# Optimization experiments

Measured on AMD Instinct MI355X. Metric: run time of the kernel, lower is better.

The kernel has to match this reference:

```python
import jax, jax.numpy as jnp
from jax import lax
import numpy as np
import math

IMPOSSIBLE = -10000.0
B, S, D_MODEL, TAG = 64, 1024, 512, 48

def setup_inputs():
    key = jax.random.key(0)
    k1, k2, k3, k4 = jax.random.split(key, 4)
    feature_vec = jax.random.normal(k1, (B, S, D_MODEL), jnp.float32)
    y = jax.random.randint(k2, (B, S), 0, TAG, dtype=jnp.int32)
    mask = jnp.zeros((B, S), dtype=bool)  # True = pad
    W = jax.random.normal(k3, (TAG, D_MODEL), jnp.float32) / math.sqrt(D_MODEL)  # feature2tag weight (out,in)
    transition = jax.random.normal(k4, (TAG + 2, TAG + 2), jnp.float32)
    transition = transition.at[:, TAG].set(IMPOSSIBLE).at[TAG + 1, :].set(IMPOSSIBLE)
    return {"feature_vec": feature_vec, "y": y, "mask": mask, "W": W, "transition": transition}

def _loss(feature_vec, W, transition, y, mask):
    b, s, d = feature_vec.shape
    t = W.shape[0]
    tag_vec = jnp.einsum('bsd,td->bst', feature_vec, W) / jnp.sqrt(jnp.float32(d))
    bm = (~mask).astype(tag_vec.dtype)                 # 1 where valid, 0 where pad
    L = (s - mask.sum(-1) - 1).astype(jnp.int32)       # last valid position per batch
    start = transition[t]                              # row SRT_IDX
    end = transition[:, t + 1]                         # col END_IDX
    trans_tt = transition[:t, :t]

    # ----- gold path score S(X, y) (fully vectorized over time) -----
    ysafe = jnp.where(mask, 0, y)
    emit = jnp.take_along_axis(tag_vec, ysafe[..., None], axis=2)[..., 0] * bm  # (b,s)
    score = start[y[:, 0]] + emit.sum(-1)
    score = score + (transition[y[:, :-1], y[:, 1:]] * bm[:, 1:]).sum(-1)
    end_tok = jnp.take_along_axis(y, L[:, None], axis=1)[:, 0]
    score = score + end[end_tok]

    # ----- log partition: forward algorithm as a fused scan over seq_len -----
    bm_next = jnp.concatenate([bm[:, 1:], jnp.zeros((b, 1), bm.dtype)], axis=1)
    def fstep(prev, inp):
        e, m0, m1 = inp  # (b,t), (b,), (b,)
        sc = (prev + e * m0[:, None])[:, :, None] + trans_tt[None] * m1[:, None, None]  # (b,t,t)
        return jax.nn.logsumexp(sc, axis=1), None
    prev0 = jnp.broadcast_to(start[:t], (b, t))
    prev, _ = lax.scan(fstep, prev0, (tag_vec.transpose(1, 0, 2), bm.T, bm_next.T))
    logZ = jax.nn.logsumexp(prev + end[:t][None], axis=-1)
    return logZ - score, tag_vec, L, trans_tt, start, end

def _viterbi(tag_vec, L, trans_tt, start, end):
    b, s, t = tag_vec.shape
    def vstep(prev, e):  # prev: (b,t,t) prev-tag x cur-tag scores; e: (b,t)
        sc = prev + e[:, None, :]
        best = sc.max(axis=1)
        idx = sc.argmax(axis=1).astype(jnp.int32)
        return best[:, :, None] + trans_tt, (best, idx)
    prev0 = jnp.broadcast_to(start[:t][None, None, :], (b, t, t))
    _, (stage_score, stage_idx) = lax.scan(vstep, prev0, tag_vec.transpose(1, 0, 2))  # (s,b,t) each
    final = stage_score[L, jnp.arange(b)] + end[:t][None]  # (b,t) scores at last valid step
    now0 = final.argmax(axis=1).astype(jnp.int32)
    # backtrace as reverse scan; padded positions emit -1
    js = jnp.arange(s - 1, 0, -1, dtype=jnp.int32)
    idx_rev = stage_idx[1:][::-1]  # step j = s-1 .. 1
    def bstep(now, inp):
        idx_j, j = inp
        prev_tag = jnp.take_along_axis(idx_j, now[:, None], axis=1)[:, 0]
        active = j <= L
        return jnp.where(active, prev_tag, now), jnp.where(active, prev_tag, -1)
    _, outs = lax.scan(bstep, now0, (idx_rev, js))  # (s-1, b): tag at position j-1
    path = jnp.concatenate([outs[::-1].T, jnp.full((b, 1), -1, jnp.int32)], axis=1)  # (b,s)
    path = path.at[jnp.arange(b), L].set(now0)
    return path

def reference(feature_vec, y, mask, W, transition):
    loss, tag_vec, L, trans_tt, start, end = _loss(feature_vec, W, transition, y, mask)
    path = _viterbi(tag_vec, L, trans_tt, start, end)
    return loss, path
```

## Files before the change

kernel.cpp:

```cpp
#include <hip/hip_runtime.h>

#define B_ 64
#define S_ 1024
#define NT 48
#define DM 512
#define TT 50

typedef float v2f __attribute__((ext_vector_type(2)));
typedef float v4f __attribute__((ext_vector_type(4)));

__global__ __launch_bounds__(256) void k_tagvec(const float* __restrict__ F,
                                                const float* __restrict__ Wm,
                                                float* __restrict__ out) {
  __shared__ float fs[128][68];
  __shared__ float wsh[48][68];
  const int t = threadIdx.x;
  const int rowBase = blockIdx.x * 128;
  const int jg = t & 3;
  const int rq = t >> 2;
  const int r0 = rq * 2, r1 = r0 + 1;
  float acc0[12];
  float acc1[12];
#pragma unroll
  for (int q = 0; q < 12; ++q) { acc0[q] = 0.f; acc1[q] = 0.f; }
  for (int kc = 0; kc < DM; kc += 64) {
    __syncthreads();
#pragma unroll
    for (int i2 = 0; i2 < 8; ++i2) {
      int f = t + i2 * 256;
      int row = f >> 4, kk = f & 15;
      float4 v = *(const float4*)(F + (size_t)(rowBase + row) * DM + kc + kk * 4);
      *(float4*)&fs[row][kk * 4] = v;
    }
#pragma unroll
    for (int i2 = 0; i2 < 3; ++i2) {
      int f = t + i2 * 256;
      int row = f >> 4, kk = f & 15;
      float4 v = *(const float4*)(Wm + (size_t)row * DM + kc + kk * 4);
      *(float4*)&wsh[row][kk * 4] = v;
    }
    __syncthreads();
#pragma unroll 4
    for (int k4 = 0; k4 < 16; ++k4) {
      float4 a0 = *(const float4*)&fs[r0][k4 * 4];
      float4 a1 = *(const float4*)&fs[r1][k4 * 4];
#pragma unroll
      for (int jj = 0; jj < 12; ++jj) {
        float4 w = *(const float4*)&wsh[jg * 12 + jj][k4 * 4];
        acc0[jj] += a0.x * w.x + a0.y * w.y + a0.z * w.z + a0.w * w.w;
        acc1[jj] += a1.x * w.x + a1.y * w.y + a1.z * w.z + a1.w * w.w;
      }
    }
  }
  const float sc = 0.044194173824159216f;
  size_t base0 = (size_t)(rowBase + r0) * NT + jg * 12;
  size_t base1 = (size_t)(rowBase + r1) * NT + jg * 12;
#pragma unroll
  for (int q = 0; q < 3; ++q) {
    float4 o0 = make_float4(acc0[q*4]*sc, acc0[q*4+1]*sc, acc0[q*4+2]*sc, acc0[q*4+3]*sc);
    float4 o1 = make_float4(acc1[q*4]*sc, acc1[q*4+1]*sc, acc1[q*4+2]*sc, acc1[q*4+3]*sc);
    *(float4*)(out + base0 + q*4) = o0;
    *(float4*)(out + base1 + q*4) = o1;
  }
}

__global__ __launch_bounds__(256) void k_score(const float* __restrict__ tg,
                                               const int* __restrict__ y,
                                               const unsigned char* __restrict__ mask,
                                               const float* __restrict__ trans,
                                               float* __restrict__ scoreOut) {
  const int b = blockIdx.x, t = threadIdx.x;
  const int* yb = y + (size_t)b * S_;
  const unsigned char* mbp = mask + (size_t)b * S_;
  float part = 0.f;
  int cnt = 0;
  for (int s = t; s < S_; s += 256) {
    int ys = yb[s];
    int ms = mbp[s];
    float bm = ms ? 0.f : 1.f;
    int yy = ms ? 0 : ys;
    part += tg[((size_t)b * S_ + s) * NT + yy] * bm;
    if (s >= 1) part += trans[yb[s - 1] * TT + ys] * bm;
    cnt += ms ? 1 : 0;
  }
  for (int d = 1; d < 64; d <<= 1) {
    part += __shfl_xor(part, d);
    cnt += __shfl_xor(cnt, d);
  }
  __shared__ float pw[4];
  __shared__ int cw[4];
  int wid = t >> 6;
  if ((t & 63) == 0) { pw[wid] = part; cw[wid] = cnt; }
  __syncthreads();
  if (t == 0) {
    float tot = pw[0] + pw[1] + pw[2] + pw[3];
    int c = cw[0] + cw[1] + cw[2] + cw[3];
    int L = S_ - 1 - c;
    tot += trans[NT * TT + yb[0]];
    tot += trans[yb[L] * TT + (NT + 1)];
    scoreOut[b] = tot;
  }
}

__global__ __launch_bounds__(64, 1) void k_scan(const float* __restrict__ tg,
                                                const unsigned char* __restrict__ mask,
                                                const float* __restrict__ trans,
                                                const float* __restrict__ score,
                                                float* __restrict__ Mbuf,
                                                int* __restrict__ nowbuf,
                                                float* __restrict__ out) {
  alignas(16) __shared__ float pls[64];
  __shared__ float bmL[S_ + 8];
  __shared__ float rbuf[256];

  const int t = threadIdx.x;
  const bool isV = blockIdx.x >= B_;
  const int b = isV ? (blockIdx.x - B_) : blockIdx.x;
  const int jc = (t < NT) ? t : (NT - 1);
  const float* tgb = tg + (size_t)b * S_ * NT;

  int cnt = 0;
  for (int m = t; m < S_; m += 64) {
    unsigned char mv = mask[(size_t)b * S_ + m];
    bmL[m] = mv ? 0.f : 1.f;
    cnt += mv ? 1 : 0;
  }
  if (t < 8) bmL[S_ + t] = 0.f;
#pragma unroll
  for (int d = 1; d < 64; d <<= 1) cnt += __shfl_xor(cnt, d);
  const int L = S_ - 1 - cnt;
  __syncthreads();

  if (!isV) {
    v2f E2[24];
#pragma unroll
    for (int q = 0; q < 24; ++q) {
      E2[q].x = __expf(trans[(2 * q) * TT + jc]);
      E2[q].y = __expf(trans[(2 * q + 1) * TT + jc]);
    }
    pls[t] = __expf(trans[NT * TT + jc] + tgb[jc] * bmL[0]);
    float ebuf[8];
#pragma unroll
    for (int k = 0; k < 8; ++k) ebuf[k] = tgb[(size_t)(k + 1) * NT + jc];
    const float* ebp = tgb + (size_t)9 * NT + jc;
    float pfinal = 0.f;

#define FSTEP(KK, RENORM, DOREFILL)                                            \
    {                                                                          \
      v4f bb4[12];                                                             \
      _Pragma("unroll")                                                        \
      for (int q = 0; q < 12; ++q) bb4[q] = *(const v4f*)&pls[4 * q];          \
      const v2f* bb = (const v2f*)bb4;                                         \
      float m1r = bmp[KK];                                                     \
      int m1b = __builtin_amdgcn_readfirstlane(__float_as_int(m1r));           \
      float Z;                                                                 \
      if (m1b != 0) {                                                          \
        v2f z0 = bb[0] * E2[0], z1 = bb[1] * E2[1];                            \
        v2f z2 = bb[2] * E2[2], z3 = bb[3] * E2[3];                            \
        _Pragma("unroll")                                                      \
        for (int q = 4; q < 24; q += 4) {                                      \
          z0 = __builtin_elementwise_fma(bb[q + 0], E2[q + 0], z0);            \
          z1 = __builtin_elementwise_fma(bb[q + 1], E2[q + 1], z1);            \
          z2 = __builtin_elementwise_fma(bb[q + 2], E2[q + 2], z2);            \
          z3 = __builtin_elementwise_fma(bb[q + 3], E2[q + 3], z3);            \
        }                                                                      \
        v2f zz = (z0 + z1) + (z2 + z3);                                        \
        Z = zz.x + zz.y;                                                       \
      } else {                                                                 \
        v2f z0 = bb[0] + bb[1], z1 = bb[2] + bb[3];                            \
        v2f z2 = bb[4] + bb[5], z3 = bb[6] + bb[7];                            \
        _Pragma("unroll")                                                      \
        for (int q = 8; q < 24; q += 4) {                                      \
          z0 = z0 + bb[q + 0]; z1 = z1 + bb[q + 1];                            \
          z2 = z2 + bb[q + 2]; z3 = z3 + bb[q + 3];                            \
        }                                                                      \
        v2f zz = (z0 + z1) + (z2 + z3);                                        \
        Z = zz.x + zz.y;                                                       \
      }                                                                        \
      float pnew = Z;                                                          \
      if (RENORM) {                                                            \
        float s48[48];                                                         \
        _Pragma("unroll")                                                      \
        for (int q = 0; q < 24; ++q) { s48[2 * q] = bb[q].x; s48[2 * q + 1] = bb[q].y; } \
        float m16[16];                                                         \
        _Pragma("unroll")                                                      \
        for (int q = 0; q < 16; ++q)                                           \
          m16[q] = fmaxf(fmaxf(s48[3 * q], s48[3 * q + 1]), s48[3 * q + 2]);   \
        float u0 = fmaxf(fmaxf(m16[0], m16[1]), m16[2]);                       \
        float u1 = fmaxf(fmaxf(m16[3], m16[4]), m16[5]);                       \
        float u2 = fmaxf(fmaxf(m16[6], m16[7]), m16[8]);                       \
        float u3 = fmaxf(fmaxf(m16[9], m16[10]), m16[11]);                     \
        float u4 = fmaxf(fmaxf(m16[12], m16[13]), m16[14]);                    \
        float w0 = fmaxf(fmaxf(u0, u1), u2);                                   \
        float w1 = fmaxf(fmaxf(u3, u4), m16[15]);                              \
        float M = fmaxf(w0, w1);                                               \
        float r = __builtin_amdgcn_rcpf(M);                                    \
        pnew = Z * r;                                                          \
        if (t == 0) rbuf[2 * g + (KK >> 2)] = r;                               \
      }                                                                        \
      float pe = pnew * __expf(ebuf[KK] * m1r);                                \
      pls[t] = pe;                                                             \
      if (DOREFILL) ebuf[KK] = ebp[KK * NT];                                   \
    }

    {
      const float* bmp = &bmL[1];
      for (int g = 0; g < 127; ++g) {
        const bool rf = (g < 126);
        FSTEP(0, 0, 1) FSTEP(1, 0, 1) FSTEP(2, 0, 1) FSTEP(3, 1, 1)
        FSTEP(4, 0, 1) FSTEP(5, 0, 1) FSTEP(6, 0, 1)
        if (rf) { FSTEP(7, 1, 1) } else { FSTEP(7, 1, 0) }
        ebp += 8 * NT;
        bmp += 8;
      }
      {
        const int g = 127;
        FSTEP(0, 0, 0) FSTEP(1, 0, 0) FSTEP(2, 0, 0) FSTEP(3, 1, 0)
        FSTEP(4, 0, 0) FSTEP(5, 0, 0) FSTEP(6, 0, 0)
      }
    }
#undef FSTEP
    {
      v4f bb4[12];
#pragma unroll
      for (int q = 0; q < 12; ++q) bb4[q] = *(const v4f*)&pls[4 * q];
      const v2f* bb = (const v2f*)bb4;
      v2f z0 = bb[0] + bb[1], z1 = bb[2] + bb[3];
      v2f z2 = bb[4] + bb[5], z3 = bb[6] + bb[7];
#pragma unroll
      for (int q = 8; q < 24; q += 4) {
        z0 = z0 + bb[q + 0]; z1 = z1 + bb[q + 1];
        z2 = z2 + bb[q + 2]; z3 = z3 + bb[q + 3];
      }
      v2f zz = (z0 + z1) + (z2 + z3);
      float Z = zz.x + zz.y;
      float s48[48];
#pragma unroll
      for (int q = 0; q < 24; ++q) { s48[2 * q] = bb[q].x; s48[2 * q + 1] = bb[q].y; }
      float m16[16];
#pragma unroll
      for (int q = 0; q < 16; ++q)
        m16[q] = fmaxf(fmaxf(s48[3 * q], s48[3 * q + 1]), s48[3 * q + 2]);
      float u0 = fmaxf(fmaxf(m16[0], m16[1]), m16[2]);
      float u1 = fmaxf(fmaxf(m16[3], m16[4]), m16[5]);
      float u2 = fmaxf(fmaxf(m16[6], m16[7]), m16[8]);
      float u3 = fmaxf(fmaxf(m16[9], m16[10]), m16[11]);
      float u4 = fmaxf(fmaxf(m16[12], m16[13]), m16[14]);
      float w0 = fmaxf(fmaxf(u0, u1), u2);
      float w1 = fmaxf(fmaxf(u3, u4), m16[15]);
      float M = fmaxf(w0, w1);
      float r = __builtin_amdgcn_rcpf(M);
      if (t == 0) rbuf[255] = r;
      pfinal = Z * r;
    }
    float ls = 0.f;
#pragma unroll
    for (int k = 0; k < 4; ++k) ls += __logf(rbuf[t + 64 * k]);
#pragma unroll
    for (int d = 1; d < 64; d <<= 1) ls += __shfl_xor(ls, d);
    float v = (t < NT) ? pfinal * __expf(trans[t * TT + (NT + 1)]) : 0.f;
#pragma unroll
    for (int d = 1; d < 64; d <<= 1) v += __shfl_xor(v, d);
    if (t == 0) out[b] = __logf(v) - ls - score[b];
  } else {
    v2f T2[24];
#pragma unroll
    for (int q = 0; q < 24; ++q) {
      T2[q].x = trans[(2 * q) * TT + jc];
      T2[q].y = trans[(2 * q + 1) * TT + jc];
    }
    float* Mb = Mbuf + (size_t)b * S_ * NT;
    const float best0 = trans[NT * TT + jc] + tgb[jc];
    pls[t] = best0;
    float ebuf[8];
#pragma unroll
    for (int k = 0; k < 8; ++k) ebuf[k] = tgb[(size_t)(1 + k) * NT + jc];
    const float* ebp = tgb + (size_t)9 * NT + jc;
    float* mbp = Mb + NT + jc;

#define VSTEP(KK, DOREFILL)                                                    \
    {                                                                          \
      v4f bb4[12];                                                             \
      _Pragma("unroll")                                                        \
      for (int q = 0; q < 12; ++q) bb4[q] = *(const v4f*)&pls[4 * q];          \
      const v2f* bb = (const v2f*)bb4;                                         \
      v2f c2[24];                                                              \
      _Pragma("unroll")                                                        \
      for (int q = 0; q < 24; ++q) c2[q] = bb[q] + T2[q];                      \
      float s48[48];                                                           \
      _Pragma("unroll")                                                        \
      for (int q = 0; q < 24; ++q) { s48[2 * q] = c2[q].x; s48[2 * q + 1] = c2[q].y; } \
      float m16[16];                                                           \
      _Pragma("unroll")                                                        \
      for (int q = 0; q < 16; ++q)                                             \
        m16[q] = fmaxf(fmaxf(s48[3 * q], s48[3 * q + 1]), s48[3 * q + 2]);     \
      float u0 = fmaxf(fmaxf(m16[0], m16[1]), m16[2]);                         \
      float u1 = fmaxf(fmaxf(m16[3], m16[4]), m16[5]);                         \
      float u2 = fmaxf(fmaxf(m16[6], m16[7]), m16[8]);                         \
      float u3 = fmaxf(fmaxf(m16[9], m16[10]), m16[11]);                       \
      float u4 = fmaxf(fmaxf(m16[12], m16[13]), m16[14]);                      \
      float w0 = fmaxf(fmaxf(u0, u1), u2);                                     \
      float w1 = fmaxf(fmaxf(u3, u4), m16[15]);                                \
      float M = fmaxf(w0, w1);                                                 \
      mbp[KK * NT] = M;                                                        \
      float bnew = M + ebuf[KK];                                               \
      pls[t] = bnew;                                                           \
      if (DOREFILL) ebuf[KK] = ebp[KK * NT];                                   \
    }

    for (int g = 0; g < 127; ++g) {
      const bool rf = (g < 126);
      VSTEP(0, 1) VSTEP(1, 1) VSTEP(2, 1) VSTEP(3, 1)
      VSTEP(4, 1) VSTEP(5, 1) VSTEP(6, 1)
      if (rf) { VSTEP(7, 1) } else { VSTEP(7, 0) }
      mbp += 8 * NT;
      ebp += 8 * NT;
    }
    VSTEP(0, 0) VSTEP(1, 0) VSTEP(2, 0) VSTEP(3, 0)
    VSTEP(4, 0) VSTEP(5, 0) VSTEP(6, 0)
#undef VSTEP
    float fin;
    if (L > 0) {
      fin = Mb[(size_t)L * NT + jc] + tgb[(size_t)L * NT + jc];
    } else {
      fin = best0;
    }
    float v = (t < NT) ? (fin + trans[t * TT + (NT + 1)]) : -3.0e38f;
    float M = v;
#pragma unroll
    for (int d = 1; d < 64; d <<= 1) M = fmaxf(M, __shfl_xor(M, d));
    unsigned long long ball = __ballot(v == M);
    int now0 = __ffsll(ball) - 1;
    if (t == 0) nowbuf[b] = now0;
  }
}

__global__ __launch_bounds__(256) void k_idx(const float* __restrict__ tg,
                                             const float* __restrict__ Mbuf,
                                             const float* __restrict__ trans,
                                             unsigned char* __restrict__ idxbuf) {
  __shared__ float TshT[NT][NT];
  const int t = threadIdx.x;
  const int b = blockIdx.x;
  for (int k = t; k < NT * NT; k += 256) {
    int i = k / NT, j = k - i * NT;
    TshT[j][i] = trans[i * TT + j];
  }
  __syncthreads();
  const int s = blockIdx.y * 128 + (t >> 1);
  const int jh = (t & 1) * 24;
  if (s < 1) return;
  const float* tgb = tg + (size_t)b * S_ * NT;
  const float* Mb = Mbuf + (size_t)b * S_ * NT;
  float bprev[NT];
  if (s == 1) {
#pragma unroll
    for (int i = 0; i < NT; ++i) bprev[i] = trans[NT * TT + i] + tgb[i];
  } else {
#pragma unroll
    for (int i = 0; i < NT; ++i)
      bprev[i] = Mb[(size_t)(s - 1) * NT + i] + tgb[(size_t)(s - 1) * NT + i];
  }
  unsigned char* ob = idxbuf + ((size_t)b * S_ + s) * NT + jh;
#pragma unroll 4
  for (int jj = 0; jj < 24; ++jj) {
    int j = jh + jj;
    float M = Mb[(size_t)s * NT + j];
    int idx = 0;
#pragma unroll
    for (int i = NT - 1; i >= 0; --i) {
      float cc = bprev[i] + TshT[j][i];
      idx = (cc == M) ? i : idx;
    }
    ob[jj] = (unsigned char)idx;
  }
}

__global__ __launch_bounds__(1024) void k_btrack(const unsigned char* __restrict__ idxbuf,
                                                 const unsigned char* __restrict__ mask,
                                                 const int* __restrict__ nowbuf,
                                                 float* __restrict__ out) {
  __shared__ unsigned char idxL[S_][NT];
  __shared__ unsigned char mapc[16][NT];
  __shared__ int ELs[16];
  __shared__ int cnt_sh;
  const int t = threadIdx.x;
  const int b = blockIdx.x;
  if (t == 0) cnt_sh = 0;
  __syncthreads();
  {
    const unsigned int* src = (const unsigned int*)(idxbuf + (size_t)b * S_ * NT);
    unsigned int* dst = (unsigned int*)&idxL[t][0];
#pragma unroll
    for (int k = 0; k < 12; ++k) dst[k] = src[(size_t)t * 12 + k];
  }
  int mv = mask[(size_t)b * S_ + t] ? 1 : 0;
  unsigned long long bal = __ballot(mv);
  int wcnt = __popcll(bal);
  if ((t & 63) == 0 && wcnt) atomicAdd(&cnt_sh, wcnt);
  __syncthreads();
  const int L = S_ - 1 - cnt_sh;
  const int now0 = nowbuf[b];
  if (t < 16 * NT) {
    const int c = t / NT;
    const int g = t - c * NT;
    int cur = g;
    const int top = (c == 15) ? (S_ - 1) : (c + 1) * 64;
    const int base = c * 64;
    for (int m = top; m > base; --m) {
      if (m <= L) cur = idxL[m][cur];
    }
    mapc[c][g] = (unsigned char)cur;
  }
  __syncthreads();
  if (t == 0) {
    int e = now0;
    ELs[15] = e;
    for (int c2 = 15; c2 >= 1; --c2) {
      e = mapc[c2][e];
      ELs[c2 - 1] = e;
    }
  }
  __syncthreads();
  float* pathOut = out + B_ + (size_t)b * S_;
  if (t < 16) {
    const int c = t;
    const int top = (c == 15) ? (S_ - 1) : (c + 1) * 64;
    const int base = c * 64;
    int cu = ELs[c];
    for (int m = top; m > base; --m) {
      if (m <= L) cu = idxL[m][cu];
      int pos = m - 1;
      pathOut[pos] = (pos > L) ? -1.0f : (float)cu;
    }
  }
  if (t == 0) pathOut[S_ - 1] = (L == S_ - 1) ? (float)now0 : -1.0f;
}

extern "C" void kernel_launch(void* const* d_in, const int* in_sizes, int n_in,
                              void* d_out, int out_size, void* d_ws, size_t ws_size,
                              hipStream_t stream) {
  const float* F = (const float*)d_in[0];
  const int* y = (const int*)d_in[1];
  const unsigned char* mask = (const unsigned char*)d_in[2];
  const float* Wm = (const float*)d_in[3];
  const float* trans = (const float*)d_in[4];
  float* out = (float*)d_out;

  const size_t NTG = (size_t)B_ * S_ * NT;
  float* tg = (float*)d_ws;
  float* score = tg + NTG;
  float* Mbuf = score + 64;
  int* nowbuf = (int*)(Mbuf + NTG);
  unsigned char* idxbuf = (unsigned char*)(nowbuf + 64);

  k_tagvec<<<dim3((B_ * S_) / 128), dim3(256), 0, stream>>>(F, Wm, tg);
  k_score<<<dim3(B_), dim3(256), 0, stream>>>(tg, y, mask, trans, score);
  k_scan<<<dim3(2 * B_), dim3(64), 0, stream>>>(tg, mask, trans, score, Mbuf, nowbuf, out);
  k_idx<<<dim3(B_, 8), dim3(256), 0, stream>>>(tg, Mbuf, trans, idxbuf);
  k_btrack<<<dim3(B_), dim3(1024), 0, stream>>>(idxbuf, mask, nowbuf, out);
}
```

Measured before the change: 318.0 us.

## Fuse gold-path score into forward scan and hoist emission loads in steps

```diff
diff --git a/kernel.cpp b/kernel.cpp
--- a/kernel.cpp
+++ b/kernel.cpp
@@ -64,61 +64,53 @@
   }
 }
 
-__global__ __launch_bounds__(256) void k_score(const float* __restrict__ tg,
-                                               const int* __restrict__ y,
-                                               const unsigned char* __restrict__ mask,
-                                               const float* __restrict__ trans,
-                                               float* __restrict__ scoreOut) {
-  const int b = blockIdx.x, t = threadIdx.x;
-  const int* yb = y + (size_t)b * S_;
-  const unsigned char* mbp = mask + (size_t)b * S_;
-  float part = 0.f;
-  int cnt = 0;
-  for (int s = t; s < S_; s += 256) {
-    int ys = yb[s];
-    int ms = mbp[s];
-    float bm = ms ? 0.f : 1.f;
-    int yy = ms ? 0 : ys;
-    part += tg[((size_t)b * S_ + s) * NT + yy] * bm;
-    if (s >= 1) part += trans[yb[s - 1] * TT + ys] * bm;
-    cnt += ms ? 1 : 0;
-  }
-  for (int d = 1; d < 64; d <<= 1) {
-    part += __shfl_xor(part, d);
-    cnt += __shfl_xor(cnt, d);
-  }
-  __shared__ float pw[4];
-  __shared__ int cw[4];
-  int wid = t >> 6;
-  if ((t & 63) == 0) { pw[wid] = part; cw[wid] = cnt; }
-  __syncthreads();
-  if (t == 0) {
-    float tot = pw[0] + pw[1] + pw[2] + pw[3];
-    int c = cw[0] + cw[1] + cw[2] + cw[3];
-    int L = S_ - 1 - c;
-    tot += trans[NT * TT + yb[0]];
-    tot += trans[yb[L] * TT + (NT + 1)];
-    scoreOut[b] = tot;
-  }
-}
-
-__global__ __launch_bounds__(64, 1) void k_scan(const float* __restrict__ tg,
-                                                const unsigned char* __restrict__ mask,
-                                                const float* __restrict__ trans,
-                                                const float* __restrict__ score,
-                                                float* __restrict__ Mbuf,
-                                                int* __restrict__ nowbuf,
-                                                float* __restrict__ out) {
+__global__ __launch_bounds__(128, 1) void k_scan(const float* __restrict__ tg,
+                                                 const int* __restrict__ y,
+                                                 const unsigned char* __restrict__ mask,
+                                                 const float* __restrict__ trans,
+                                                 float* __restrict__ Mbuf,
+                                                 int* __restrict__ nowbuf,
+                                                 float* __restrict__ out) {
   alignas(16) __shared__ float pls[64];
   __shared__ float bmL[S_ + 8];
   __shared__ float rbuf[256];
+  __shared__ float sc_lds;
 
   const int t = threadIdx.x;
   const bool isV = blockIdx.x >= B_;
   const int b = isV ? (blockIdx.x - B_) : blockIdx.x;
+  const float* tgb = tg + (size_t)b * S_ * NT;
+
+  if (t >= 64) {
+    if (!isV) {
+      const int* yb = y + (size_t)b * S_;
+      const unsigned char* mbp2 = mask + (size_t)b * S_;
+      float part = 0.f;
+      int cnt = 0;
+      for (int s = t - 64; s < S_; s += 64) {
+        int ys = yb[s];
+        int ms = mbp2[s];
+        float bm = ms ? 0.f : 1.f;
+        int yy = ms ? 0 : ys;
+        part += tgb[(size_t)s * NT + yy] * bm;
+        if (s >= 1) part += trans[yb[s - 1] * TT + ys] * bm;
+        cnt += ms ? 1 : 0;
+      }
+#pragma unroll
+      for (int d = 1; d < 64; d <<= 1) {
+        part += __shfl_xor(part, d);
+        cnt += __shfl_xor(cnt, d);
+      }
+      if ((t & 63) == 0) {
+        int L2 = S_ - 1 - cnt;
+        sc_lds = part + trans[NT * TT + yb[0]] + trans[yb[L2] * TT + (NT + 1)];
+      }
+    }
+    __syncthreads();
+    return;
+  }
+
   const int jc = (t < NT) ? t : (NT - 1);
-  const float* tgb = tg + (size_t)b * S_ * NT;
-
   int cnt = 0;
   for (int m = t; m < S_; m += 64) {
     unsigned char mv = mask[(size_t)b * S_ + m];
@@ -150,6 +142,8 @@
       v4f bb4[12];                                                             \
       _Pragma("unroll")                                                        \
       for (int q = 0; q < 12; ++q) bb4[q] = *(const v4f*)&pls[4 * q];          \
+      float ev = ebuf[KK];                                                     \
+      if (DOREFILL) ebuf[KK] = ebp[KK * NT];  \
       const v2f* bb = (const v2f*)bb4;                                         \
       float m1r = bmp[KK];                                                     \
       int m1b = __builtin_amdgcn_readfirstlane(__float_as_int(m1r));           \
@@ -198,9 +192,8 @@
         pnew = Z * r;                                                          \
         if (t == 0) rbuf[2 * g + (KK >> 2)] = r;                               \
       }                                                                        \
-      float pe = pnew * __expf(ebuf[KK] * m1r);                                \
+      float pe = pnew * __expf(ev * m1r);                                      \
       pls[t] = pe;                                                             \
-      if (DOREFILL) ebuf[KK] = ebp[KK * NT];                                   \
     }
 
     {
@@ -215,6 +208,7 @@
       }
       {
         const int g = 127;
+        const float* bmp = &bmL[1017];
         FSTEP(0, 0, 0) FSTEP(1, 0, 0) FSTEP(2, 0, 0) FSTEP(3, 1, 0)
         FSTEP(4, 0, 0) FSTEP(5, 0, 0) FSTEP(6, 0, 0)
       }
@@ -261,7 +255,7 @@
     float v = (t < NT) ? pfinal * __expf(trans[t * TT + (NT + 1)]) : 0.f;
 #pragma unroll
     for (int d = 1; d < 64; d <<= 1) v += __shfl_xor(v, d);
-    if (t == 0) out[b] = __logf(v) - ls - score[b];
+    if (t == 0) out[b] = __logf(v) - ls - sc_lds;
   } else {
     v2f T2[24];
 #pragma unroll
@@ -272,6 +266,7 @@
     float* Mb = Mbuf + (size_t)b * S_ * NT;
     const float best0 = trans[NT * TT + jc] + tgb[jc];
     pls[t] = best0;
+    float Mprev = best0;
     float ebuf[8];
 #pragma unroll
     for (int k = 0; k < 8; ++k) ebuf[k] = tgb[(size_t)(1 + k) * NT + jc];
@@ -283,6 +278,9 @@
       v4f bb4[12];                                                             \
       _Pragma("unroll")                                                        \
       for (int q = 0; q < 12; ++q) bb4[q] = *(const v4f*)&pls[4 * q];          \
+      mbp[(KK - 1) * NT] = Mprev;               \
+      float ev = ebuf[KK];                                                     \
+      if (DOREFILL) ebuf[KK] = ebp[KK * NT];           \
       const v2f* bb = (const v2f*)bb4;                                         \
       v2f c2[24];                                                              \
       _Pragma("unroll")                                                        \
@@ -302,10 +300,9 @@
       float w0 = fmaxf(fmaxf(u0, u1), u2);                                     \
       float w1 = fmaxf(fmaxf(u3, u4), m16[15]);                                \
       float M = fmaxf(w0, w1);                                                 \
-      mbp[KK * NT] = M;                                                        \
-      float bnew = M + ebuf[KK];                                               \
+      float bnew = M + ev;                                                     \
       pls[t] = bnew;                                                           \
-      if (DOREFILL) ebuf[KK] = ebp[KK * NT];                                   \
+      Mprev = M;                                                               \
     }
 
     for (int g = 0; g < 127; ++g) {
@@ -319,6 +316,7 @@
     VSTEP(0, 0) VSTEP(1, 0) VSTEP(2, 0) VSTEP(3, 0)
     VSTEP(4, 0) VSTEP(5, 0) VSTEP(6, 0)
 #undef VSTEP
+    mbp[6 * NT] = Mprev;
     float fin;
     if (L > 0) {
       fin = Mb[(size_t)L * NT + jc] + tgb[(size_t)L * NT + jc];
@@ -449,14 +447,12 @@
 
   const size_t NTG = (size_t)B_ * S_ * NT;
   float* tg = (float*)d_ws;
-  float* score = tg + NTG;
-  float* Mbuf = score + 64;
+  float* Mbuf = tg + NTG;
   int* nowbuf = (int*)(Mbuf + NTG);
   unsigned char* idxbuf = (unsigned char*)(nowbuf + 64);
 
   k_tagvec<<<dim3((B_ * S_) / 128), dim3(256), 0, stream>>>(F, Wm, tg);
-  k_score<<<dim3(B_), dim3(256), 0, stream>>>(tg, y, mask, trans, score);
-  k_scan<<<dim3(2 * B_), dim3(64), 0, stream>>>(tg, mask, trans, score, Mbuf, nowbuf, out);
+  k_scan<<<dim3(2 * B_), dim3(128), 0, stream>>>(tg, y, mask, trans, Mbuf, nowbuf, out);
   k_idx<<<dim3(B_, 8), dim3(256), 0, stream>>>(tg, Mbuf, trans, idxbuf);
   k_btrack<<<dim3(B_), dim3(1024), 0, stream>>>(idxbuf, mask, nowbuf, out);
 }
```

New measurement: 325.2 us. 1.02x slower.

## Fuse gold-score, argmax-index and backtrack kernels into one per-batch kernel

Applied to the files above, without the earlier changes.

```diff
diff --git a/kernel.cpp b/kernel.cpp
--- a/kernel.cpp
+++ b/kernel.cpp
@@ -64,48 +64,9 @@
   }
 }
 
-__global__ __launch_bounds__(256) void k_score(const float* __restrict__ tg,
-                                               const int* __restrict__ y,
-                                               const unsigned char* __restrict__ mask,
-                                               const float* __restrict__ trans,
-                                               float* __restrict__ scoreOut) {
-  const int b = blockIdx.x, t = threadIdx.x;
-  const int* yb = y + (size_t)b * S_;
-  const unsigned char* mbp = mask + (size_t)b * S_;
-  float part = 0.f;
-  int cnt = 0;
-  for (int s = t; s < S_; s += 256) {
-    int ys = yb[s];
-    int ms = mbp[s];
-    float bm = ms ? 0.f : 1.f;
-    int yy = ms ? 0 : ys;
-    part += tg[((size_t)b * S_ + s) * NT + yy] * bm;
-    if (s >= 1) part += trans[yb[s - 1] * TT + ys] * bm;
-    cnt += ms ? 1 : 0;
-  }
-  for (int d = 1; d < 64; d <<= 1) {
-    part += __shfl_xor(part, d);
-    cnt += __shfl_xor(cnt, d);
-  }
-  __shared__ float pw[4];
-  __shared__ int cw[4];
-  int wid = t >> 6;
-  if ((t & 63) == 0) { pw[wid] = part; cw[wid] = cnt; }
-  __syncthreads();
-  if (t == 0) {
-    float tot = pw[0] + pw[1] + pw[2] + pw[3];
-    int c = cw[0] + cw[1] + cw[2] + cw[3];
-    int L = S_ - 1 - c;
-    tot += trans[NT * TT + yb[0]];
-    tot += trans[yb[L] * TT + (NT + 1)];
-    scoreOut[b] = tot;
-  }
-}
-
 __global__ __launch_bounds__(64, 1) void k_scan(const float* __restrict__ tg,
                                                 const unsigned char* __restrict__ mask,
                                                 const float* __restrict__ trans,
-                                                const float* __restrict__ score,
                                                 float* __restrict__ Mbuf,
                                                 int* __restrict__ nowbuf,
                                                 float* __restrict__ out) {
@@ -261,7 +222,7 @@
     float v = (t < NT) ? pfinal * __expf(trans[t * TT + (NT + 1)]) : 0.f;
 #pragma unroll
     for (int d = 1; d < 64; d <<= 1) v += __shfl_xor(v, d);
-    if (t == 0) out[b] = __logf(v) - ls - score[b];
+    if (t == 0) out[b] = __logf(v) - ls;
   } else {
     v2f T2[24];
 #pragma unroll
@@ -335,69 +296,102 @@
   }
 }
 
-__global__ __launch_bounds__(256) void k_idx(const float* __restrict__ tg,
-                                             const float* __restrict__ Mbuf,
-                                             const float* __restrict__ trans,
-                                             unsigned char* __restrict__ idxbuf) {
+__global__ __launch_bounds__(1024) void k_idxbt(const float* __restrict__ tg,
+                                                const float* __restrict__ Mbuf,
+                                                const int* __restrict__ y,
+                                                const unsigned char* __restrict__ mask,
+                                                const float* __restrict__ trans,
+                                                const int* __restrict__ nowbuf,
+                                                float* __restrict__ out) {
   __shared__ float TshT[NT][NT];
-  const int t = threadIdx.x;
-  const int b = blockIdx.x;
-  for (int k = t; k < NT * NT; k += 256) {
-    int i = k / NT, j = k - i * NT;
-    TshT[j][i] = trans[i * TT + j];
-  }
-  __syncthreads();
-  const int s = blockIdx.y * 128 + (t >> 1);
-  const int jh = (t & 1) * 24;
-  if (s < 1) return;
-  const float* tgb = tg + (size_t)b * S_ * NT;
-  const float* Mb = Mbuf + (size_t)b * S_ * NT;
-  float bprev[NT];
-  if (s == 1) {
-#pragma unroll
-    for (int i = 0; i < NT; ++i) bprev[i] = trans[NT * TT + i] + tgb[i];
-  } else {
-#pragma unroll
-    for (int i = 0; i < NT; ++i)
-      bprev[i] = Mb[(size_t)(s - 1) * NT + i] + tgb[(size_t)(s - 1) * NT + i];
-  }
-  unsigned char* ob = idxbuf + ((size_t)b * S_ + s) * NT + jh;
-#pragma unroll 4
-  for (int jj = 0; jj < 24; ++jj) {
-    int j = jh + jj;
-    float M = Mb[(size_t)s * NT + j];
-    int idx = 0;
-#pragma unroll
-    for (int i = NT - 1; i >= 0; --i) {
-      float cc = bprev[i] + TshT[j][i];
-      idx = (cc == M) ? i : idx;
-    }
-    ob[jj] = (unsigned char)idx;
-  }
-}
-
-__global__ __launch_bounds__(1024) void k_btrack(const unsigned char* __restrict__ idxbuf,
-                                                 const unsigned char* __restrict__ mask,
-                                                 const int* __restrict__ nowbuf,
-                                                 float* __restrict__ out) {
   __shared__ unsigned char idxL[S_][NT];
   __shared__ unsigned char mapc[16][NT];
   __shared__ int ELs[16];
   __shared__ int cnt_sh;
+  __shared__ float pw[4];
+  __shared__ int cw[4];
+  __shared__ float sc_sh;
+
   const int t = threadIdx.x;
   const int b = blockIdx.x;
+  const float* tgb = tg + (size_t)b * S_ * NT;
+  const float* Mb = Mbuf + (size_t)b * S_ * NT;
   if (t == 0) cnt_sh = 0;
-  __syncthreads();
-  {
-    const unsigned int* src = (const unsigned int*)(idxbuf + (size_t)b * S_ * NT);
-    unsigned int* dst = (unsigned int*)&idxL[t][0];
-#pragma unroll
-    for (int k = 0; k < 12; ++k) dst[k] = src[(size_t)t * 12 + k];
+  for (int k = t; k < NT * NT; k += 1024) {
+    int i = k / NT, j = k - i * NT;
+    TshT[j][i] = trans[i * TT + j];
   }
   int mv = mask[(size_t)b * S_ + t] ? 1 : 0;
   unsigned long long bal = __ballot(mv);
   int wcnt = __popcll(bal);
   if ((t & 63) == 0 && wcnt) atomicAdd(&cnt_sh, wcnt);
+  if (t < 256) {
+    const int* yb = y + (size_t)b * S_;
+    const unsigned char* mbp = mask + (size_t)b * S_;
+    float part = 0.f;
+    int cnt = 0;
+    for (int s = t; s < S_; s += 256) {
+      int ys = yb[s];
+      int ms = mbp[s];
+      float bm = ms ? 0.f : 1.f;
+      int yy = ms ? 0 : ys;
+      part += tgb[(size_t)s * NT + yy] * bm;
+      if (s >= 1) part += trans[yb[s - 1] * TT + ys] * bm;
+      cnt += ms ? 1 : 0;
+    }
+#pragma unroll
+    for (int d = 1; d < 64; d <<= 1) {
+      part += __shfl_xor(part, d);
+      cnt += __shfl_xor(cnt, d);
+    }
+    int wid = t >> 6;
+    if ((t & 63) == 0) { pw[wid] = part; cw[wid] = cnt; }
+  }
+  __syncthreads();
+  if (t == 0) {
+    float tot = pw[0] + pw[1] + pw[2] + pw[3];
+    int c = cw[0] + cw[1] + cw[2] + cw[3];
+    int L2 = S_ - 1 - c;
+    const int* yb = y + (size_t)b * S_;
+    sc_sh = tot + trans[NT * TT + yb[0]] + trans[yb[L2] * TT + (NT + 1)];
+  }
+  if (t >= 1) {
+    const int s = t;
+    float bprev[NT];
+    if (s == 1) {
+#pragma unroll
+      for (int i = 0; i < NT; ++i) bprev[i] = trans[NT * TT + i] + tgb[i];
+    } else {
+#pragma unroll
+      for (int q = 0; q < 12; ++q) {
+        float4 mm = *(const float4*)(Mb + (size_t)(s - 1) * NT + 4 * q);
+        float4 ee = *(const float4*)(tgb + (size_t)(s - 1) * NT + 4 * q);
+        bprev[4 * q + 0] = mm.x + ee.x;
+        bprev[4 * q + 1] = mm.y + ee.y;
+        bprev[4 * q + 2] = mm.z + ee.z;
+        bprev[4 * q + 3] = mm.w + ee.w;
+      }
+    }
+    unsigned int* dst = (unsigned int*)&idxL[s][0];
+#pragma unroll 3
+    for (int jw = 0; jw < 12; ++jw) {
+      float4 Mv = *(const float4*)(Mb + (size_t)s * NT + 4 * jw);
+      unsigned int pk = 0;
+#pragma unroll
+      for (int jj = 0; jj < 4; ++jj) {
+        int j = 4 * jw + jj;
+        float M = (jj == 0) ? Mv.x : (jj == 1) ? Mv.y : (jj == 2) ? Mv.z : Mv.w;
+        int idx = 0;
+#pragma unroll
+        for (int i = NT - 1; i >= 0; --i) {
+          float cc = bprev[i] + TshT[j][i];
+          idx = (cc == M) ? i : idx;
+        }
+        pk |= ((unsigned int)idx) << (8 * jj);
+      }
+      dst[jw] = pk;
+    }
+  }
   __syncthreads();
   const int L = S_ - 1 - cnt_sh;
   const int now0 = nowbuf[b];
@@ -434,7 +428,10 @@
       pathOut[pos] = (pos > L) ? -1.0f : (float)cu;
     }
   }
-  if (t == 0) pathOut[S_ - 1] = (L == S_ - 1) ? (float)now0 : -1.0f;
+  if (t == 0) {
+    pathOut[S_ - 1] = (L == S_ - 1) ? (float)now0 : -1.0f;
+    out[b] = out[b] - sc_sh;
+  }
 }
 
 extern "C" void kernel_launch(void* const* d_in, const int* in_sizes, int n_in,
@@ -449,14 +446,10 @@
 
   const size_t NTG = (size_t)B_ * S_ * NT;
   float* tg = (float*)d_ws;
-  float* score = tg + NTG;
-  float* Mbuf = score + 64;
+  float* Mbuf = tg + NTG;
   int* nowbuf = (int*)(Mbuf + NTG);
-  unsigned char* idxbuf = (unsigned char*)(nowbuf + 64);
 
   k_tagvec<<<dim3((B_ * S_) / 128), dim3(256), 0, stream>>>(F, Wm, tg);
-  k_score<<<dim3(B_), dim3(256), 0, stream>>>(tg, y, mask, trans, score);
-  k_scan<<<dim3(2 * B_), dim3(64), 0, stream>>>(tg, mask, trans, score, Mbuf, nowbuf, out);
-  k_idx<<<dim3(B_, 8), dim3(256), 0, stream>>>(tg, Mbuf, trans, idxbuf);
-  k_btrack<<<dim3(B_), dim3(1024), 0, stream>>>(idxbuf, mask, nowbuf, out);
+  k_scan<<<dim3(2 * B_), dim3(64), 0, stream>>>(tg, mask, trans, Mbuf, nowbuf, out);
+  k_idxbt<<<dim3(B_), dim3(1024), 0, stream>>>(tg, Mbuf, y, mask, trans, nowbuf, out);
 }
```

Result: slower. 364.6 us (+14.6%).
